# Optimization experiments

Hardware: AMD Instinct MI355X
Metric: run time of the kernel (lower is better)

Reference implementation:

```python
import jax, jax.numpy as jnp
import numpy as np

HEIGHT = 108
WIDTH = 108
LEN_CLASSES = 7
EPS = 1e-5


def layout_bbox(pred, H, W):
    # pred: [B, O, 4 + LEN_CLASSES]
    bbox = pred[..., :4]
    cls_prob = pred[..., 4:]  # [B,O,7]
    x_c = bbox[..., 0] * W   # [B,O]
    y_c = bbox[..., 1] * H
    w = bbox[..., 2] * W
    h = bbox[..., 3] * H
    x1 = (x_c - 0.5 * w)[:, :, None, None]  # [B,O,1,1]
    x2 = (x_c + 0.5 * w)[:, :, None, None]
    y1 = (y_c - 0.5 * h)[:, :, None, None]
    y2 = (y_c + 0.5 * h)[:, :, None, None]
    xt = jnp.arange(W, dtype=pred.dtype)[None, None, None, :]  # [1,1,1,W]
    yt = jnp.arange(H, dtype=pred.dtype)[None, None, :, None]  # [1,1,H,1]
    x1d = xt - x1  # [B,O,1,W]
    x2d = x2 - xt
    y1d = yt - y1  # [B,O,H,1]
    y2d = y2 - yt
    # min(relu(d), 1) == clip(d, 0, 1)
    yband = jnp.clip(y1d, 0.0, 1.0) * jnp.clip(y2d, 0.0, 1.0)  # [B,O,H,1]
    xband = jnp.clip(x1d, 0.0, 1.0) * jnp.clip(x2d, 0.0, 1.0)  # [B,O,1,W]
    x1_line = jax.nn.relu(1.0 - jnp.abs(x1d)) * yband  # [B,O,H,W]
    x2_line = jax.nn.relu(1.0 - jnp.abs(x2d)) * yband
    y1_line = jax.nn.relu(1.0 - jnp.abs(y1d)) * xband
    y2_line = jax.nn.relu(1.0 - jnp.abs(y2d)) * xband
    xy_max = jnp.maximum(jnp.maximum(x1_line, x2_line), jnp.maximum(y1_line, y2_line))  # [B,O,H,W]
    spatial = xy_max[..., None] * cls_prob[:, :, None, None, :]  # [B,O,H,W,7]
    return jnp.max(spatial, axis=1)  # [B,H,W,7]


def bn(x, g, b, axes):
    m = jnp.mean(x, axis=axes, keepdims=True)
    v = jnp.var(x, axis=axes, keepdims=True)
    shape = [1] * x.ndim
    shape[1 if x.ndim == 4 else -1] = -1
    return (x - m) * jax.lax.rsqrt(v + EPS) * g.reshape(shape) + b.reshape(shape)


def conv2d(x, w, b, stride):
    y = jax.lax.conv_general_dilated(x, w, (stride, stride), 'VALID',
                                     dimension_numbers=('NCHW', 'OIHW', 'NCHW'))
    return y + b[None, :, None, None]


def setup_inputs() -> dict:
    key = jax.random.key(0)
    ks = jax.random.split(key, 16)
    B, O = 64, 16
    d = {}
    d['image'] = jax.random.uniform(ks[0], (B, O, 4 + LEN_CLASSES), dtype=jnp.float32)
    d['conv1_w'] = jax.random.normal(ks[1], (32, LEN_CLASSES, 5, 5), jnp.float32) * 0.05
    d['conv1_b'] = jnp.zeros((32,), jnp.float32)
    d['bn1_g'] = jnp.ones((32,), jnp.float32)
    d['bn1_b'] = jnp.zeros((32,), jnp.float32)
    d['conv2_w'] = jax.random.normal(ks[2], (64, 32, 5, 5), jnp.float32) * 0.03
    d['conv2_b'] = jnp.zeros((64,), jnp.float32)
    d['bn2_g'] = jnp.ones((64,), jnp.float32)
    d['bn2_b'] = jnp.zeros((64,), jnp.float32)
    d['fc1_w'] = jax.random.normal(ks[3], (512, 36864), jnp.float32) * 0.005
    d['fc1_b'] = jnp.zeros((512,), jnp.float32)
    d['bn3_g'] = jnp.ones((512,), jnp.float32)
    d['bn3_b'] = jnp.zeros((512,), jnp.float32)
    d['fc2_w'] = jax.random.normal(ks[4], (1, 512), jnp.float32) * 0.04
    d['fc2_b'] = jnp.zeros((1,), jnp.float32)
    return d


def reference(image, conv1_w, conv1_b, bn1_g, bn1_b, conv2_w, conv2_b, bn2_g, bn2_b,
              fc1_w, fc1_b, bn3_g, bn3_b, fc2_w, fc2_b):
    # layout_bbox(image, WIDTH, HEIGHT): output_height=WIDTH, output_width=HEIGHT (both 108)
    layout = layout_bbox(image, WIDTH, HEIGHT)           # [B,108,108,7]
    x = jnp.transpose(layout, (0, 3, 1, 2))              # [B,7,108,108]
    x = conv2d(x, conv1_w, conv1_b, 2)                   # [B,32,52,52]
    x = bn(x, bn1_g, bn1_b, (0, 2, 3))
    x = jax.nn.leaky_relu(x, 0.2)
    x = conv2d(x, conv2_w, conv2_b, 2)                   # [B,64,24,24]
    x = bn(x, bn2_g, bn2_b, (0, 2, 3))
    x = jax.nn.leaky_relu(x, 0.2)
    x = x.reshape(x.shape[0], -1)                        # [B,36864]
    x = x @ fc1_w.T + fc1_b                              # [B,512]
    x = bn(x, bn3_g, bn3_b, (0,))
    x = jax.nn.leaky_relu(x, 0.2)
    x = x @ fc2_w.T + fc2_b                              # [B,1]
    return jax.nn.sigmoid(x)
```

## Files before the change

### kernel.cpp

```cpp
#include <hip/hip_runtime.h>
#include <hip/hip_bf16.h>


typedef unsigned short u16;
typedef __attribute__((ext_vector_type(8))) short bf8_t;
typedef __attribute__((ext_vector_type(4))) float f4_t;
#define MFMA16(a, b, c) __builtin_amdgcn_mfma_f32_16x16x32_bf16(a, b, c, 0, 0, 0)

#define LEAKY(v) (fmaxf((v), 0.2f * (v)))
#define CLIP01(v) fminf(fmaxf((v), 0.0f), 1.0f)

__device__ inline unsigned f2bf(float f) {
  unsigned u = __float_as_uint(f);
  return (u + 0x7FFFu + ((u >> 16) & 1u)) >> 16;
}

constexpr int HW = 108;
constexpr int NOBJ = 16;
constexpr int NCLS = 7;

__global__ __launch_bounds__(128) void layout_kernel(
    const float* __restrict__ image, u16* __restrict__ lay8) {
  int h = blockIdx.x, b = blockIdx.y;
  __shared__ float sIm[NOBJ * 11];
  int tid = threadIdx.x;
  for (int i = tid; i < NOBJ * 11; i += 128) sIm[i] = image[b * NOBJ * 11 + i];
  __syncthreads();
  int w = tid;
  if (w >= HW) return;
  float best[NCLS];
#pragma unroll
  for (int c = 0; c < NCLS; ++c) best[c] = 0.0f;
  float fw = (float)w, fh = (float)h;
  for (int o = 0; o < NOBJ; ++o) {
    const float* p = &sIm[o * 11];
    float xc = p[0] * 108.0f, yc = p[1] * 108.0f;
    float wd = p[2] * 108.0f, hd = p[3] * 108.0f;
    float x1 = xc - 0.5f * wd, x2 = xc + 0.5f * wd;
    float y1 = yc - 0.5f * hd, y2 = yc + 0.5f * hd;
    float x1d = fw - x1, x2d = x2 - fw;
    float y1d = fh - y1, y2d = y2 - fh;
    float yband = CLIP01(y1d) * CLIP01(y2d);
    float xband = CLIP01(x1d) * CLIP01(x2d);
    float x1l = fmaxf(1.0f - fabsf(x1d), 0.0f) * yband;
    float x2l = fmaxf(1.0f - fabsf(x2d), 0.0f) * yband;
    float y1l = fmaxf(1.0f - fabsf(y1d), 0.0f) * xband;
    float y2l = fmaxf(1.0f - fabsf(y2d), 0.0f) * xband;
    float xy = fmaxf(fmaxf(x1l, x2l), fmaxf(y1l, y2l));
#pragma unroll
    for (int c = 0; c < NCLS; ++c) best[c] = fmaxf(best[c], xy * p[4 + c]);
  }
  unsigned p0 = f2bf(best[0]) | (f2bf(best[1]) << 16);
  unsigned p1 = f2bf(best[2]) | (f2bf(best[3]) << 16);
  unsigned p2 = f2bf(best[4]) | (f2bf(best[5]) << 16);
  unsigned p3 = f2bf(best[6]);
  uint4 st = {p0, p1, p2, p3};
  ((uint4*)lay8)[b * 11664 + h * 108 + w] = st;
}

__global__ __launch_bounds__(256) void wprep1_kernel(
    const float* __restrict__ w1, u16* __restrict__ wB1) {
  int i = blockIdx.x * 256 + threadIdx.x;
  int co = i / 224, k = i % 224;
  int chunk = k >> 5, kk = k & 31, tl = kk >> 3, ci = kk & 7;
  int tap = chunk * 4 + tl;
  unsigned v = 0;
  if (tap < 25 && ci < 7) v = f2bf(w1[co * 175 + ci * 25 + tap]);
  wB1[i] = (u16)v;
}
__global__ __launch_bounds__(256) void wprep2_kernel(
    const float* __restrict__ w2, u16* __restrict__ wB2) {
  int i = blockIdx.x * 256 + threadIdx.x;
  int tap = i / 2048, r = i % 2048, co = r >> 5, ci = r & 31;
  wB2[i] = (u16)f2bf(w2[co * 800 + ci * 25 + tap]);
}

__global__ __launch_bounds__(128) void conv1_mfma(
    const u16* __restrict__ lay8, const u16* __restrict__ wB1,
    float* __restrict__ x1c) {
  int strip = blockIdx.x, b = blockIdx.y;
  int tid = threadIdx.x;
  int lane = tid & 63, wv = tid >> 6;
  int f = lane & 15, q = lane >> 4;
  int co = wv * 16 + f;
  int pbase[13];
#pragma unroll
  for (int t = 0; t < 13; ++t) {
    int P = strip * 208 + t * 16 + f;
    int oh = P / 52, ow = P - oh * 52;
    pbase[t] = (oh * 2 * 108 + ow * 2) * 8;
  }
  const u16* lb = lay8 + (size_t)b * 93312;
  f4_t acc[13];
#pragma unroll
  for (int t = 0; t < 13; ++t) acc[t] = {0.f, 0.f, 0.f, 0.f};
#pragma unroll
  for (int chunk = 0; chunk < 7; ++chunk) {
    int tap = chunk * 4 + q;
    tap = tap > 24 ? 24 : tap;
    int kh = tap / 5, kw = tap - kh * 5;
    int toff = (kh * 108 + kw) * 8;
    bf8_t bf = *(const bf8_t*)&wB1[co * 224 + chunk * 32 + q * 8];
    bf8_t af[13];
#pragma unroll
    for (int t = 0; t < 13; ++t) af[t] = *(const bf8_t*)&lb[pbase[t] + toff];
#pragma unroll
    for (int t = 0; t < 13; ++t) acc[t] = MFMA16(af[t], bf, acc[t]);
  }
  float* ob = x1c + (size_t)b * 2704 * 32;
#pragma unroll
  for (int t = 0; t < 13; ++t) {
#pragma unroll
    for (int r = 0; r < 4; ++r) {
      int P = strip * 208 + t * 16 + q * 4 + r;
      ob[P * 32 + co] = acc[t][r];
    }
  }
}

__global__ __launch_bounds__(256) void stats_c_kernel(
    const float* __restrict__ src, int C, int logC,
    float* __restrict__ sumP, float* __restrict__ sqP) {
  int t = threadIdx.x;
  int c = t & (C - 1);
  int rl = t >> logC;
  int rpi = 256 >> logC;
  const float* p = src + (size_t)blockIdx.x * 256 * C;
  float s = 0.f, q = 0.f;
  for (int it = 0; it < C; ++it) {
    float v = p[(it * rpi + rl) * C + c];
    s += v;
    q += v * v;
  }
  __shared__ float ls[256], lq[256];
  ls[t] = s;
  lq[t] = q;
  __syncthreads();
  if (t < C) {
    float ss = 0.f, qq = 0.f;
    for (int j = t; j < 256; j += C) { ss += ls[j]; qq += lq[j]; }
    atomicAdd(&sumP[t], ss);
    atomicAdd(&sqP[t], qq);
  }
}

__global__ void bn_finalize_kernel(
    const float* __restrict__ sum, const float* __restrict__ sumsq,
    const float* __restrict__ g, const float* __restrict__ bb, float invN,
    int C, float* __restrict__ scale, float* __restrict__ shift) {
  int c = threadIdx.x;
  if (c < C) {
    float mean = sum[c] * invN;
    float var = sumsq[c] * invN - mean * mean;
    float sc = g[c] * rsqrtf(var + 1e-5f);
    scale[c] = sc;
    shift[c] = bb[c] - mean * sc;
  }
}

__global__ __launch_bounds__(256) void bnapply1_kernel(
    const float* __restrict__ x1c, const float* __restrict__ sc,
    const float* __restrict__ sh, u16* __restrict__ x1b) {
  int idx = blockIdx.x * 256 + threadIdx.x;
  int base = idx * 8, c0 = base & 31;
  float4 v0 = *(const float4*)&x1c[base];
  float4 v1 = *(const float4*)&x1c[base + 4];
  float o[8] = {v0.x, v0.y, v0.z, v0.w, v1.x, v1.y, v1.z, v1.w};
  unsigned out[4];
#pragma unroll
  for (int j = 0; j < 4; ++j) {
    float a = LEAKY(fmaf(o[2 * j], sc[c0 + 2 * j], sh[c0 + 2 * j]));
    float bq = LEAKY(fmaf(o[2 * j + 1], sc[c0 + 2 * j + 1], sh[c0 + 2 * j + 1]));
    out[j] = f2bf(a) | (f2bf(bq) << 16);
  }
  uint4 st = {out[0], out[1], out[2], out[3]};
  *(uint4*)&x1b[base] = st;
}

__global__ __launch_bounds__(256) void conv2_mfma(
    const u16* __restrict__ x1b, const u16* __restrict__ wB2,
    float* __restrict__ x2c) {
  int strip = blockIdx.x, b = blockIdx.y;
  int tid = threadIdx.x;
  int lane = tid & 63, wv = tid >> 6;
  int f = lane & 15, q = lane >> 4;
  int mbase = (wv >> 1) * 3, nbase = (wv & 1) * 2;
  int pbase[3];
#pragma unroll
  for (int t = 0; t < 3; ++t) {
    int P = strip * 96 + (mbase + t) * 16 + f;
    int oh = P / 24, ow = P - oh * 24;
    pbase[t] = (oh * 2 * 52 + ow * 2) * 32 + q * 8;
  }
  const u16* xb = x1b + (size_t)b * 86528;
  f4_t acc[3][2];
#pragma unroll
  for (int t = 0; t < 3; ++t)
#pragma unroll
    for (int n = 0; n < 2; ++n) acc[t][n] = {0.f, 0.f, 0.f, 0.f};
#pragma unroll
  for (int tap = 0; tap < 25; ++tap) {
    int kh = tap / 5, kw = tap - kh * 5;
    int toff = (kh * 52 + kw) * 32;
    bf8_t bfr[2];
#pragma unroll
    for (int n = 0; n < 2; ++n)
      bfr[n] = *(const bf8_t*)&wB2[tap * 2048 + ((nbase + n) * 16 + f) * 32 + q * 8];
    bf8_t afr[3];
#pragma unroll
    for (int t = 0; t < 3; ++t) afr[t] = *(const bf8_t*)&xb[pbase[t] + toff];
#pragma unroll
    for (int t = 0; t < 3; ++t)
#pragma unroll
      for (int n = 0; n < 2; ++n) acc[t][n] = MFMA16(afr[t], bfr[n], acc[t][n]);
  }
  float* ob = x2c + (size_t)b * 576 * 64;
#pragma unroll
  for (int t = 0; t < 3; ++t)
#pragma unroll
    for (int n = 0; n < 2; ++n)
#pragma unroll
      for (int r = 0; r < 4; ++r) {
        int P = strip * 96 + (mbase + t) * 16 + q * 4 + r;
        ob[P * 64 + (nbase + n) * 16 + f] = acc[t][n][r];
      }
}

__global__ __launch_bounds__(256) void bnapply2t_kernel(
    const float* __restrict__ x2c, const float* __restrict__ sc2,
    const float* __restrict__ sh2, u16* __restrict__ xB) {
  int hw0 = blockIdx.x * 64, b = blockIdx.y;
  __shared__ float tile[64 * 65];
  int t = threadIdx.x;
  int c = t & 63, hl4 = t >> 6;
  float s = sc2[c], h = sh2[c];
#pragma unroll
  for (int it = 0; it < 16; ++it) {
    int hl = it * 4 + hl4;
    float v = x2c[((size_t)b * 576 + hw0 + hl) * 64 + c];
    tile[hl * 65 + c] = LEAKY(fmaf(v, s, h));
  }
  __syncthreads();
  int hw = t & 63, cl4 = t >> 6;
#pragma unroll
  for (int it = 0; it < 16; ++it) {
    int cc = it * 4 + cl4;
    xB[(size_t)b * 36864 + cc * 576 + hw0 + hw] = (u16)f2bf(tile[hw * 65 + cc]);
  }
}

__global__ __launch_bounds__(256) void fc1_mfma(
    const u16* __restrict__ xB, const float* __restrict__ wgt,
    float* __restrict__ part) {
  int ks = blockIdx.x, nb = blockIdx.y;
  int tid = threadIdx.x;
  int lane = tid & 63, wv = tid >> 6;
  int f = lane & 15, q = lane >> 4;
  int n0 = nb * 64 + wv * 16;
  __shared__ u16 sA[64 * 32];
  f4_t acc[4];
#pragma unroll
  for (int m = 0; m < 4; ++m) acc[m] = {0.f, 0.f, 0.f, 0.f};
  int kbase = ks * 1024;
  for (int kt = 0; kt < 32; ++kt) {
    int k0 = kbase + kt * 32;
    __syncthreads();
    *(uint4*)&sA[(tid >> 2) * 32 + (tid & 3) * 8] =
        *(const uint4*)&xB[(size_t)(tid >> 2) * 36864 + k0 + (tid & 3) * 8];
    __syncthreads();
    const float* wp = wgt + (size_t)(n0 + f) * 36864 + k0 + q * 8;
    float4 wa = *(const float4*)wp;
    float4 wb = *(const float4*)(wp + 4);
    union { bf8_t v; u16 u[8]; } bu;
    bu.u[0] = (u16)f2bf(wa.x); bu.u[1] = (u16)f2bf(wa.y);
    bu.u[2] = (u16)f2bf(wa.z); bu.u[3] = (u16)f2bf(wa.w);
    bu.u[4] = (u16)f2bf(wb.x); bu.u[5] = (u16)f2bf(wb.y);
    bu.u[6] = (u16)f2bf(wb.z); bu.u[7] = (u16)f2bf(wb.w);
    bf8_t afr[4];
#pragma unroll
    for (int m = 0; m < 4; ++m)
      afr[m] = *(const bf8_t*)&sA[(m * 16 + f) * 32 + q * 8];
#pragma unroll
    for (int m = 0; m < 4; ++m) acc[m] = MFMA16(afr[m], bu.v, acc[m]);
  }
  float* pp = part + (size_t)ks * 32768;
#pragma unroll
  for (int m = 0; m < 4; ++m)
#pragma unroll
    for (int r = 0; r < 4; ++r)
      pp[(m * 16 + q * 4 + r) * 512 + n0 + f] = acc[m][r];
}

__global__ __launch_bounds__(256) void fc1_reduce_kernel(
    const float* __restrict__ part, float* __restrict__ out) {
  int i = blockIdx.x * 256 + threadIdx.x;
  float s = 0.f;
#pragma unroll 4
  for (int ks = 0; ks < 36; ++ks) s += part[(size_t)ks * 32768 + i];
  out[i] = s;
}

__global__ __launch_bounds__(64) void bn3_kernel(
    const float* __restrict__ fc1o, const float* __restrict__ g,
    const float* __restrict__ bb, float* __restrict__ scale,
    float* __restrict__ shift) {
  int f = blockIdx.x * 64 + threadIdx.x;
  float s = 0.f, q = 0.f;
  for (int m = 0; m < 64; ++m) {
    float v = fc1o[m * 512 + f];
    s += v;
    q += v * v;
  }
  float mean = s * (1.f / 64.f);
  float var = q * (1.f / 64.f) - mean * mean;
  float sc = g[f] * rsqrtf(var + 1e-5f);
  scale[f] = sc;
  shift[f] = bb[f] - mean * sc;
}

__global__ __launch_bounds__(64) void fc2_kernel(
    const float* __restrict__ fc1o, const float* __restrict__ sc,
    const float* __restrict__ sh, const float* __restrict__ w2,
    const float* __restrict__ b2, float* __restrict__ out) {
  int m = blockIdx.x;
  int f = threadIdx.x;
  float acc = 0.f;
#pragma unroll
  for (int j = 0; j < 8; ++j) {
    int ff = f + j * 64;
    float v = fc1o[m * 512 + ff] * sc[ff] + sh[ff];
    v = LEAKY(v);
    acc += v * w2[ff];
  }
  for (int off = 32; off; off >>= 1) acc += __shfl_down(acc, off, 64);
  if (f == 0) out[m] = 1.f / (1.f + expf(-(acc + b2[0])));
}

extern "C" void kernel_launch(void* const* d_in, const int* in_sizes, int n_in,
                              void* d_out, int out_size, void* d_ws,
                              size_t ws_size, hipStream_t stream) {
  const float* image = (const float*)d_in[0];
  const float* c1w = (const float*)d_in[1];
  const float* bn1g = (const float*)d_in[3];
  const float* bn1b = (const float*)d_in[4];
  const float* c2w = (const float*)d_in[5];
  const float* bn2g = (const float*)d_in[7];
  const float* bn2b = (const float*)d_in[8];
  const float* f1w = (const float*)d_in[9];
  const float* bn3g = (const float*)d_in[11];
  const float* bn3b = (const float*)d_in[12];
  const float* f2w = (const float*)d_in[13];
  const float* f2b = (const float*)d_in[14];
  float* ws = (float*)d_ws;

  u16* lay8 = (u16*)ws;
  u16* x1b = (u16*)ws;
  float* x1c = ws + 2985984;
  float* x2c = ws + 2985984;
  u16* xB = (u16*)(ws + 5345280);
  float* fc1part = ws + 6524928;
  float* fc1o = ws + 8523776;
  float* st = ws + 8556544;
  float* bn1sum = st, *bn1sq = st + 32, *bn2sum = st + 64, *bn2sq = st + 128;
  float* coef = ws + 8556736;
  float* sc1 = coef, *sh1 = coef + 32;
  float* sc2 = coef + 64, *sh2 = coef + 128;
  float* sc3 = coef + 192, *sh3 = coef + 704;
  u16* wB1 = (u16*)(ws + 8557952);
  u16* wB2 = (u16*)(ws + 8561536);

  hipMemsetAsync(st, 0, 192 * sizeof(float), stream);

  wprep1_kernel<<<28, 256, 0, stream>>>(c1w, wB1);
  wprep2_kernel<<<200, 256, 0, stream>>>(c2w, wB2);
  layout_kernel<<<dim3(108, 64), 128, 0, stream>>>(image, lay8);
  conv1_mfma<<<dim3(13, 64), 128, 0, stream>>>(lay8, wB1, x1c);
  stats_c_kernel<<<676, 256, 0, stream>>>(x1c, 32, 5, bn1sum, bn1sq);
  bn_finalize_kernel<<<1, 64, 0, stream>>>(bn1sum, bn1sq, bn1g, bn1b,
                                           1.f / 173056.f, 32, sc1, sh1);
  bnapply1_kernel<<<2704, 256, 0, stream>>>(x1c, sc1, sh1, x1b);
  conv2_mfma<<<dim3(6, 64), 256, 0, stream>>>(x1b, wB2, x2c);
  stats_c_kernel<<<144, 256, 0, stream>>>(x2c, 64, 6, bn2sum, bn2sq);
  bn_finalize_kernel<<<1, 64, 0, stream>>>(bn2sum, bn2sq, bn2g, bn2b,
                                           1.f / 36864.f, 64, sc2, sh2);
  bnapply2t_kernel<<<dim3(9, 64), 256, 0, stream>>>(x2c, sc2, sh2, xB);
  fc1_mfma<<<dim3(36, 8), 256, 0, stream>>>(xB, f1w, fc1part);
  fc1_reduce_kernel<<<128, 256, 0, stream>>>(fc1part, fc1o);
  bn3_kernel<<<8, 64, 0, stream>>>(fc1o, bn3g, bn3b, sc3, sh3);
  fc2_kernel<<<64, 64, 0, stream>>>(fc1o, sc3, sh3, f2w, f2b, (float*)d_out);
}
```

Baseline: 297.1 us.

## Fuse BN statistics into conv epilogues, store conv1 as bf16, restage fc1 split-K

BatchNorm sum and sum-of-squares are now accumulated in the conv1 and conv2 epilogues with wave shuffles and atomics, which removes both stats_c passes over the activations. The conv1 output is stored as bf16 instead of fp32, halving its write and its re-read in bnapply1. The two weight-prep kernels are merged into one launch. fc1 uses twice as many split-K blocks, each staging its whole 512-wide A slice into shared memory once instead of syncing per k-step. The costs are bf16 rounding before normalization, more atomic contention on the BN accumulators, and more partial sums to reduce.

```diff
diff --git a/kernel.cpp b/kernel.cpp
--- a/kernel.cpp
+++ b/kernel.cpp
@@ -13,6 +13,9 @@
 __device__ inline unsigned f2bf(float f) {
   unsigned u = __float_as_uint(f);
   return (u + 0x7FFFu + ((u >> 16) & 1u)) >> 16;
+}
+__device__ inline float bf2f(unsigned u) {
+  return __uint_as_float(u << 16);
 }
 
 constexpr int HW = 108;
@@ -58,26 +61,28 @@
   ((uint4*)lay8)[b * 11664 + h * 108 + w] = st;
 }
 
-__global__ __launch_bounds__(256) void wprep1_kernel(
-    const float* __restrict__ w1, u16* __restrict__ wB1) {
+__global__ __launch_bounds__(256) void wprep_kernel(
+    const float* __restrict__ w1, const float* __restrict__ w2,
+    u16* __restrict__ wB1, u16* __restrict__ wB2) {
   int i = blockIdx.x * 256 + threadIdx.x;
-  int co = i / 224, k = i % 224;
-  int chunk = k >> 5, kk = k & 31, tl = kk >> 3, ci = kk & 7;
-  int tap = chunk * 4 + tl;
-  unsigned v = 0;
-  if (tap < 25 && ci < 7) v = f2bf(w1[co * 175 + ci * 25 + tap]);
-  wB1[i] = (u16)v;
-}
-__global__ __launch_bounds__(256) void wprep2_kernel(
-    const float* __restrict__ w2, u16* __restrict__ wB2) {
-  int i = blockIdx.x * 256 + threadIdx.x;
-  int tap = i / 2048, r = i % 2048, co = r >> 5, ci = r & 31;
-  wB2[i] = (u16)f2bf(w2[co * 800 + ci * 25 + tap]);
+  if (i < 7168) {
+    int co = i / 224, k = i % 224;
+    int chunk = k >> 5, kk = k & 31, tl = kk >> 3, ci = kk & 7;
+    int tap = chunk * 4 + tl;
+    unsigned v = 0;
+    if (tap < 25 && ci < 7) v = f2bf(w1[co * 175 + ci * 25 + tap]);
+    wB1[i] = (u16)v;
+  } else {
+    int j = i - 7168;
+    int tap = j / 2048, r = j % 2048, co = r >> 5, ci = r & 31;
+    wB2[j] = (u16)f2bf(w2[co * 800 + ci * 25 + tap]);
+  }
 }
 
 __global__ __launch_bounds__(128) void conv1_mfma(
     const u16* __restrict__ lay8, const u16* __restrict__ wB1,
-    float* __restrict__ x1c) {
+    u16* __restrict__ x1r, float* __restrict__ bn1sum,
+    float* __restrict__ bn1sq) {
   int strip = blockIdx.x, b = blockIdx.y;
   int tid = threadIdx.x;
   int lane = tid & 63, wv = tid >> 6;
@@ -107,40 +112,26 @@
 #pragma unroll
     for (int t = 0; t < 13; ++t) acc[t] = MFMA16(af[t], bf, acc[t]);
   }
-  float* ob = x1c + (size_t)b * 2704 * 32;
+  u16* ob = x1r + (size_t)b * 86528;
+  float s = 0.f, sq = 0.f;
 #pragma unroll
   for (int t = 0; t < 13; ++t) {
 #pragma unroll
     for (int r = 0; r < 4; ++r) {
+      float v = acc[t][r];
+      s += v;
+      sq += v * v;
       int P = strip * 208 + t * 16 + q * 4 + r;
-      ob[P * 32 + co] = acc[t][r];
+      ob[P * 32 + co] = (u16)f2bf(v);
     }
   }
-}
-
-__global__ __launch_bounds__(256) void stats_c_kernel(
-    const float* __restrict__ src, int C, int logC,
-    float* __restrict__ sumP, float* __restrict__ sqP) {
-  int t = threadIdx.x;
-  int c = t & (C - 1);
-  int rl = t >> logC;
-  int rpi = 256 >> logC;
-  const float* p = src + (size_t)blockIdx.x * 256 * C;
-  float s = 0.f, q = 0.f;
-  for (int it = 0; it < C; ++it) {
-    float v = p[(it * rpi + rl) * C + c];
-    s += v;
-    q += v * v;
-  }
-  __shared__ float ls[256], lq[256];
-  ls[t] = s;
-  lq[t] = q;
-  __syncthreads();
-  if (t < C) {
-    float ss = 0.f, qq = 0.f;
-    for (int j = t; j < 256; j += C) { ss += ls[j]; qq += lq[j]; }
-    atomicAdd(&sumP[t], ss);
-    atomicAdd(&sqP[t], qq);
+  s += __shfl_xor(s, 16);
+  s += __shfl_xor(s, 32);
+  sq += __shfl_xor(sq, 16);
+  sq += __shfl_xor(sq, 32);
+  if (lane < 16) {
+    atomicAdd(&bn1sum[co], s);
+    atomicAdd(&bn1sq[co], sq);
   }
 }
 
@@ -159,18 +150,19 @@
 }
 
 __global__ __launch_bounds__(256) void bnapply1_kernel(
-    const float* __restrict__ x1c, const float* __restrict__ sc,
+    const u16* __restrict__ x1r, const float* __restrict__ sc,
     const float* __restrict__ sh, u16* __restrict__ x1b) {
   int idx = blockIdx.x * 256 + threadIdx.x;
   int base = idx * 8, c0 = base & 31;
-  float4 v0 = *(const float4*)&x1c[base];
-  float4 v1 = *(const float4*)&x1c[base + 4];
-  float o[8] = {v0.x, v0.y, v0.z, v0.w, v1.x, v1.y, v1.z, v1.w};
+  uint4 in = *(const uint4*)&x1r[base];
+  unsigned w[4] = {in.x, in.y, in.z, in.w};
   unsigned out[4];
 #pragma unroll
   for (int j = 0; j < 4; ++j) {
-    float a = LEAKY(fmaf(o[2 * j], sc[c0 + 2 * j], sh[c0 + 2 * j]));
-    float bq = LEAKY(fmaf(o[2 * j + 1], sc[c0 + 2 * j + 1], sh[c0 + 2 * j + 1]));
+    float a = bf2f(w[j] & 0xffffu);
+    float bq = bf2f(w[j] >> 16);
+    a = LEAKY(fmaf(a, sc[c0 + 2 * j], sh[c0 + 2 * j]));
+    bq = LEAKY(fmaf(bq, sc[c0 + 2 * j + 1], sh[c0 + 2 * j + 1]));
     out[j] = f2bf(a) | (f2bf(bq) << 16);
   }
   uint4 st = {out[0], out[1], out[2], out[3]};
@@ -179,7 +171,8 @@
 
 __global__ __launch_bounds__(256) void conv2_mfma(
     const u16* __restrict__ x1b, const u16* __restrict__ wB2,
-    float* __restrict__ x2c) {
+    float* __restrict__ x2c, float* __restrict__ bn2sum,
+    float* __restrict__ bn2sq) {
   int strip = blockIdx.x, b = blockIdx.y;
   int tid = threadIdx.x;
   int lane = tid & 63, wv = tid >> 6;
@@ -205,7 +198,8 @@
     bf8_t bfr[2];
 #pragma unroll
     for (int n = 0; n < 2; ++n)
-      bfr[n] = *(const bf8_t*)&wB2[tap * 2048 + ((nbase + n) * 16 + f) * 32 + q * 8];
+      bfr[n] =
+          *(const bf8_t*)&wB2[tap * 2048 + ((nbase + n) * 16 + f) * 32 + q * 8];
     bf8_t afr[3];
 #pragma unroll
     for (int t = 0; t < 3; ++t) afr[t] = *(const bf8_t*)&xb[pbase[t] + toff];
@@ -215,15 +209,34 @@
       for (int n = 0; n < 2; ++n) acc[t][n] = MFMA16(afr[t], bfr[n], acc[t][n]);
   }
   float* ob = x2c + (size_t)b * 576 * 64;
+  float s[2] = {0.f, 0.f}, sq[2] = {0.f, 0.f};
 #pragma unroll
   for (int t = 0; t < 3; ++t)
 #pragma unroll
     for (int n = 0; n < 2; ++n)
 #pragma unroll
       for (int r = 0; r < 4; ++r) {
+        float v = acc[t][n][r];
+        s[n] += v;
+        sq[n] += v * v;
         int P = strip * 96 + (mbase + t) * 16 + q * 4 + r;
-        ob[P * 64 + (nbase + n) * 16 + f] = acc[t][n][r];
+        ob[P * 64 + (nbase + n) * 16 + f] = v;
       }
+#pragma unroll
+  for (int n = 0; n < 2; ++n) {
+    s[n] += __shfl_xor(s[n], 16);
+    s[n] += __shfl_xor(s[n], 32);
+    sq[n] += __shfl_xor(sq[n], 16);
+    sq[n] += __shfl_xor(sq[n], 32);
+  }
+  if (lane < 16) {
+#pragma unroll
+    for (int n = 0; n < 2; ++n) {
+      int c = (nbase + n) * 16 + f;
+      atomicAdd(&bn2sum[c], s[n]);
+      atomicAdd(&bn2sq[c], sq[n]);
+    }
+  }
 }
 
 __global__ __launch_bounds__(256) void bnapply2t_kernel(
@@ -257,18 +270,23 @@
   int lane = tid & 63, wv = tid >> 6;
   int f = lane & 15, q = lane >> 4;
   int n0 = nb * 64 + wv * 16;
-  __shared__ u16 sA[64 * 32];
+  int kbase = ks * 512;
+  __shared__ u16 sA[64 * 520];
+#pragma unroll
+  for (int i = 0; i < 16; ++i) {
+    int c = i * 256 + tid;
+    int row = c >> 6, col = c & 63;
+    *(uint4*)&sA[row * 520 + col * 8] =
+        *(const uint4*)&xB[(size_t)row * 36864 + kbase + col * 8];
+  }
+  __syncthreads();
   f4_t acc[4];
 #pragma unroll
   for (int m = 0; m < 4; ++m) acc[m] = {0.f, 0.f, 0.f, 0.f};
-  int kbase = ks * 1024;
-  for (int kt = 0; kt < 32; ++kt) {
-    int k0 = kbase + kt * 32;
-    __syncthreads();
-    *(uint4*)&sA[(tid >> 2) * 32 + (tid & 3) * 8] =
-        *(const uint4*)&xB[(size_t)(tid >> 2) * 36864 + k0 + (tid & 3) * 8];
-    __syncthreads();
-    const float* wp = wgt + (size_t)(n0 + f) * 36864 + k0 + q * 8;
+  const float* wrow = wgt + (size_t)(n0 + f) * 36864 + kbase + q * 8;
+#pragma unroll 4
+  for (int kt = 0; kt < 16; ++kt) {
+    const float* wp = wrow + kt * 32;
     float4 wa = *(const float4*)wp;
     float4 wb = *(const float4*)(wp + 4);
     union { bf8_t v; u16 u[8]; } bu;
@@ -279,7 +297,7 @@
     bf8_t afr[4];
 #pragma unroll
     for (int m = 0; m < 4; ++m)
-      afr[m] = *(const bf8_t*)&sA[(m * 16 + f) * 32 + q * 8];
+      afr[m] = *(const bf8_t*)&sA[(m * 16 + f) * 520 + kt * 32 + q * 8];
 #pragma unroll
     for (int m = 0; m < 4; ++m) acc[m] = MFMA16(afr[m], bu.v, acc[m]);
   }
@@ -295,8 +313,8 @@
     const float* __restrict__ part, float* __restrict__ out) {
   int i = blockIdx.x * 256 + threadIdx.x;
   float s = 0.f;
-#pragma unroll 4
-  for (int ks = 0; ks < 36; ++ks) s += part[(size_t)ks * 32768 + i];
+#pragma unroll 8
+  for (int ks = 0; ks < 72; ++ks) s += part[(size_t)ks * 32768 + i];
   out[i] = s;
 }
 
@@ -355,36 +373,33 @@
 
   u16* lay8 = (u16*)ws;
   u16* x1b = (u16*)ws;
-  float* x1c = ws + 2985984;
+  u16* x1r = (u16*)(ws + 2985984);
   float* x2c = ws + 2985984;
+  float* fc1part = ws + 2985984;
   u16* xB = (u16*)(ws + 5345280);
-  float* fc1part = ws + 6524928;
-  float* fc1o = ws + 8523776;
-  float* st = ws + 8556544;
+  float* fc1o = ws + 6524928;
+  float* st = ws + 6557696;
   float* bn1sum = st, *bn1sq = st + 32, *bn2sum = st + 64, *bn2sq = st + 128;
-  float* coef = ws + 8556736;
+  float* coef = ws + 6557888;
   float* sc1 = coef, *sh1 = coef + 32;
   float* sc2 = coef + 64, *sh2 = coef + 128;
   float* sc3 = coef + 192, *sh3 = coef + 704;
-  u16* wB1 = (u16*)(ws + 8557952);
-  u16* wB2 = (u16*)(ws + 8561536);
+  u16* wB1 = (u16*)(ws + 6559104);
+  u16* wB2 = (u16*)(ws + 6562688);
 
   hipMemsetAsync(st, 0, 192 * sizeof(float), stream);
 
-  wprep1_kernel<<<28, 256, 0, stream>>>(c1w, wB1);
-  wprep2_kernel<<<200, 256, 0, stream>>>(c2w, wB2);
+  wprep_kernel<<<228, 256, 0, stream>>>(c1w, c2w, wB1, wB2);
   layout_kernel<<<dim3(108, 64), 128, 0, stream>>>(image, lay8);
-  conv1_mfma<<<dim3(13, 64), 128, 0, stream>>>(lay8, wB1, x1c);
-  stats_c_kernel<<<676, 256, 0, stream>>>(x1c, 32, 5, bn1sum, bn1sq);
+  conv1_mfma<<<dim3(13, 64), 128, 0, stream>>>(lay8, wB1, x1r, bn1sum, bn1sq);
   bn_finalize_kernel<<<1, 64, 0, stream>>>(bn1sum, bn1sq, bn1g, bn1b,
                                            1.f / 173056.f, 32, sc1, sh1);
-  bnapply1_kernel<<<2704, 256, 0, stream>>>(x1c, sc1, sh1, x1b);
-  conv2_mfma<<<dim3(6, 64), 256, 0, stream>>>(x1b, wB2, x2c);
-  stats_c_kernel<<<144, 256, 0, stream>>>(x2c, 64, 6, bn2sum, bn2sq);
+  bnapply1_kernel<<<2704, 256, 0, stream>>>(x1r, sc1, sh1, x1b);
+  conv2_mfma<<<dim3(6, 64), 256, 0, stream>>>(x1b, wB2, x2c, bn2sum, bn2sq);
   bn_finalize_kernel<<<1, 64, 0, stream>>>(bn2sum, bn2sq, bn2g, bn2b,
                                            1.f / 36864.f, 64, sc2, sh2);
   bnapply2t_kernel<<<dim3(9, 64), 256, 0, stream>>>(x2c, sc2, sh2, xB);
-  fc1_mfma<<<dim3(36, 8), 256, 0, stream>>>(xB, f1w, fc1part);
+  fc1_mfma<<<dim3(72, 8), 256, 0, stream>>>(xB, f1w, fc1part);
   fc1_reduce_kernel<<<128, 256, 0, stream>>>(fc1part, fc1o);
   bn3_kernel<<<8, 64, 0, stream>>>(fc1o, bn3g, bn3b, sc3, sh3);
   fc2_kernel<<<64, 64, 0, stream>>>(fc1o, sc3, sh3, f2w, f2b, (float*)d_out);
```

Result: faster. 256.4 us (-13.7%).
